# Optimization experiments

Measured on AMD Instinct MI355X. Metric: run time of the kernel, lower is better.

Reference implementation:

```python
import jax, jax.numpy as jnp
import numpy as np

H, W = 256, 256
S, S_IDX, END_BIAS = 48, 3, 10
E_IDX = S - END_BIAS          # 38
N_ITER = E_IDX - (S_IDX + 1)  # 34 sequential segments after the start segment
OUT_WIN = 10                  # outlier1d window length
OUT_THRESH = 2.0


def setup_inputs() -> dict:
    key = jax.random.key(0)
    # (x, y) event coordinates in [0, W) x [0, H); t/p/b columns are unused by the module.
    events = jax.random.uniform(key, (16, 960000, 2), jnp.float32, minval=0.0, maxval=256.0)
    return {"events": events}


def _blur(a):
    """5x5 uniform (0.04) blur, SAME padding; a: [B, S, D] -> [B, S, D]."""
    k = jnp.full((1, 1, 5, 5), 0.04, jnp.float32)
    return jax.lax.conv_general_dilated(a[:, None], k, (1, 1), [(2, 2), (2, 2)])[:, 0]


def _outlier_flags(m):
    """outlier1d(m[b, si:si+10], thresh=2)[0] for si in [S_IDX+1, E_IDX). m: [B,S] -> bool [B,N_ITER]."""
    widx = (jnp.arange(N_ITER)[:, None] + S_IDX + 1) + jnp.arange(OUT_WIN)[None, :]
    w = m[:, widx]                                   # [B, N_ITER, 10]
    med = jnp.median(w, axis=-1, keepdims=True)
    diff = jnp.abs(w - med)
    mad = jnp.median(diff, axis=-1)                  # [B, N_ITER]
    return 0.6745 * diff[..., 0] / mad > OUT_THRESH


def reference(events):
    B, N, _ = events.shape
    segmentLen = N // S            # static python int
    Nu = segmentLen * S
    x = events[:, :Nu, 0].astype(jnp.int32)   # [B, Nu]
    y = events[:, :Nu, 1].astype(jnp.int32)
    chunks = jnp.repeat(jnp.arange(S), segmentLen)   # segment id per event, [Nu]
    bidx = jnp.arange(B)[:, None]

    # per-batch x-t / y-t histograms via scatter-add
    alongX = jnp.zeros((B, S, W), jnp.float32).at[bidx, chunks[None, :], x].add(1.0)
    alongY = jnp.zeros((B, S, H), jnp.float32).at[bidx, chunks[None, :], y].add(1.0)

    def proc_axis(along, D):
        flat = along.reshape(B, -1)
        cv = (flat.mean(-1) + 3.0 * jnp.std(flat, axis=-1, ddof=1))[:, None, None]
        a = _blur(jnp.clip(along, 0.0, cv))
        m = jnp.einsum('bsd,d->bs', a, jnp.arange(D, dtype=jnp.float32)) / segmentLen
        start = m[:, S_IDX:S_IDX + 1]
        aligned = jnp.round(m - start - (D // 2 - start)).astype(jnp.int32)
        return m, aligned

    meanX, alignedX = proc_axis(alongX, W)
    meanY, alignedY = proc_axis(alongY, H)
    is_out = _outlier_flags(meanX) | _outlier_flags(meanY)   # [B, N_ITER]

    def per_batch(xb, yb, aX, aY, outb):
        xs = jnp.clip(xb - aX[chunks], 0, W - 1)
        ys = jnp.clip(yb - aY[chunks], 0, H - 1)
        idx_c = (xs + W * ys).reshape(S, segmentLen)
        idx_v = (xs // 2 + (W // 2) * (ys // 2)).reshape(S, segmentLen)
        container0 = jnp.zeros(W * H, jnp.int32).at[idx_c[S_IDX]].add(1)
        ver0 = jnp.zeros((W // 2) * (H // 2), bool).at[idx_v[S_IDX]].set(True)

        def step(carry, inp):
            container, ver, stopped = carry
            ic, iv, is_o = inp
            ver_new = ver.at[iv].set(True)
            cnt = jnp.sum(ver_new).astype(jnp.float32)
            new_info = jnp.sum(jnp.logical_xor(ver_new, ver)).astype(jnp.float32)
            brk = new_info / cnt < 0.1
            do = (~stopped) & (~is_o) & (~brk)
            stopped = stopped | ((~stopped) & (~is_o) & brk)
            container = jnp.where(do, container.at[ic].add(1), container)
            ver = jnp.where(do, ver_new, ver)
            return (container, ver, stopped), None

        (container, _, _), _ = jax.lax.scan(
            step, (container0, ver0, jnp.array(False)),
            (idx_c[S_IDX + 1:E_IDX], idx_v[S_IDX + 1:E_IDX], outb))
        c = container.astype(jnp.float32)
        cv = c.mean() + 3.0 * jnp.std(c, ddof=1)
        return jnp.clip(c, 0.0, cv) / cv

    containers = jax.vmap(per_batch)(x, y, alignedX, alignedY, is_out)  # [B, W*H]
    return containers.reshape(B, 1, H, W)
```

## Files before the change

kernel.cpp:

```cpp
#include <hip/hip_runtime.h>

#define NB 16
#define NEV 960000
#define NS 48
#define SEG 20000
#define S_IDX 3
#define E_IDX 38
#define N_ITER 34
#define ND 256
#define NCH 35

__device__ inline void centroid_pl(const float* __restrict__ along,
                                   float cv, int sI, int lane,
                                   float* mf_out, int* ai_out) {
    float vals[4][5];
    #pragma unroll
    for (int k = 0; k < 4; ++k) {
        int d = lane + 64 * k;
        #pragma unroll
        for (int ds = -2; ds <= 2; ++ds) {
            int ss = sI + ds;
            vals[k][ds + 2] = (ss >= 0 && ss < NS) ? along[ss * ND + d] : 0.0f;
        }
    }
    double acc = 0.0;
    #pragma unroll
    for (int k = 0; k < 4; ++k) {
        int d = lane + 64 * k;
        int lo = d - 2 < 0 ? 0 : d - 2;
        int hi = d + 2 > 255 ? 255 : d + 2;
        double Wd = 0.5 * (double)(lo + hi) * (double)(hi - lo + 1);
        double t = 0.0;
        #pragma unroll
        for (int ds = -2; ds <= 2; ++ds) {
            int ss = sI + ds;
            if (ss >= 0 && ss < NS) t += (double)fminf(vals[k][ds + 2], cv);
        }
        acc += t * Wd;
    }
    for (int off = 32; off; off >>= 1) acc += __shfl_down(acc, off);
    float mf = (float)(acc * 0.04 / (double)SEG);
    *mf_out = mf;
    *ai_out = (int)rintf(mf - 128.0f);
}

__device__ inline float cv_from_sums(const unsigned long long* __restrict__ cvsums,
                                     int b, int axis) {
    double ts  = 960000.0;
    double ts2 = (double)cvsums[b * 2 + axis];
    const double N = (double)(NS * ND);
    double mean = ts / N;
    double var  = (ts2 - ts * ts / N) / (N - 1.0);
    return (float)(mean + 3.0 * sqrt(var));
}

__global__ __launch_bounds__(256) void hist_kernel(const float* __restrict__ events,
                                                   float* __restrict__ alongX,
                                                   float* __restrict__ alongY,
                                                   unsigned* __restrict__ compact,
                                                   unsigned* __restrict__ container,
                                                   unsigned* __restrict__ masks,
                                                   unsigned long long* __restrict__ cvsums) {
    __shared__ unsigned hx[4][ND], hy[4][ND];
    __shared__ unsigned long long qredX[4], qredY[4];
    int tid = threadIdx.x;
    int blk = blockIdx.x;
    int b = blk / NS, c = blk % NS;
    int wave = tid >> 6, lane = tid & 63;
    #pragma unroll
    for (int j = 0; j < 4; j++) { hx[j][tid] = 0; hy[j][tid] = 0; }
    {
        uint4 z = {0u, 0u, 0u, 0u};
        for (int i = blk * 256 + tid; i < 262144; i += NB * NS * 256)
            ((uint4*)container)[i] = z;
        for (int i = blk * 256 + tid; i < 71680; i += NB * NS * 256)
            ((uint4*)masks)[i] = z;
        if (blk == 0 && tid < NB * 2) cvsums[tid] = 0ull;
    }
    __syncthreads();
    size_t base = (size_t)b * NEV + (size_t)c * SEG;
    const float4* ev4 = (const float4*)(events + base * 2);
    bool wr = (c >= S_IDX && c < E_IDX);
    uint4* dst = wr ? (uint4*)(compact + ((size_t)b * NCH + (c - S_IDX)) * (SEG / 2)) : nullptr;
    unsigned* HX = hx[wave];
    unsigned* HY = hy[wave];
    for (int k = tid; k < SEG / 8; k += 256) {
        float4 v0 = ev4[4 * k], v1 = ev4[4 * k + 1], v2 = ev4[4 * k + 2], v3 = ev4[4 * k + 3];
        int x0 = (int)v0.x, y0 = (int)v0.y, x1 = (int)v0.z, y1 = (int)v0.w;
        int x2 = (int)v1.x, y2 = (int)v1.y, x3 = (int)v1.z, y3 = (int)v1.w;
        int x4 = (int)v2.x, y4 = (int)v2.y, x5 = (int)v2.z, y5 = (int)v2.w;
        int x6 = (int)v3.x, y6 = (int)v3.y, x7 = (int)v3.z, y7 = (int)v3.w;
        x0 = x0 > 255 ? 255 : x0; y0 = y0 > 255 ? 255 : y0;
        x1 = x1 > 255 ? 255 : x1; y1 = y1 > 255 ? 255 : y1;
        x2 = x2 > 255 ? 255 : x2; y2 = y2 > 255 ? 255 : y2;
        x3 = x3 > 255 ? 255 : x3; y3 = y3 > 255 ? 255 : y3;
        x4 = x4 > 255 ? 255 : x4; y4 = y4 > 255 ? 255 : y4;
        x5 = x5 > 255 ? 255 : x5; y5 = y5 > 255 ? 255 : y5;
        x6 = x6 > 255 ? 255 : x6; y6 = y6 > 255 ? 255 : y6;
        x7 = x7 > 255 ? 255 : x7; y7 = y7 > 255 ? 255 : y7;
        atomicAdd(&HX[x0], 1u); atomicAdd(&HY[y0], 1u);
        atomicAdd(&HX[x1], 1u); atomicAdd(&HY[y1], 1u);
        atomicAdd(&HX[x2], 1u); atomicAdd(&HY[y2], 1u);
        atomicAdd(&HX[x3], 1u); atomicAdd(&HY[y3], 1u);
        atomicAdd(&HX[x4], 1u); atomicAdd(&HY[y4], 1u);
        atomicAdd(&HX[x5], 1u); atomicAdd(&HY[y5], 1u);
        atomicAdd(&HX[x6], 1u); atomicAdd(&HY[y6], 1u);
        atomicAdd(&HX[x7], 1u); atomicAdd(&HY[y7], 1u);
        if (wr) {
            uint4 p;
            p.x = (unsigned)(x0 | (y0 << 8)) | ((unsigned)(x1 | (y1 << 8)) << 16);
            p.y = (unsigned)(x2 | (y2 << 8)) | ((unsigned)(x3 | (y3 << 8)) << 16);
            p.z = (unsigned)(x4 | (y4 << 8)) | ((unsigned)(x5 | (y5 << 8)) << 16);
            p.w = (unsigned)(x6 | (y6 << 8)) | ((unsigned)(x7 | (y7 << 8)) << 16);
            dst[k] = p;
        }
    }
    __syncthreads();
    unsigned sx = hx[0][tid] + hx[1][tid] + hx[2][tid] + hx[3][tid];
    unsigned sy = hy[0][tid] + hy[1][tid] + hy[2][tid] + hy[3][tid];
    int o = (b * NS + c) * ND + tid;
    alongX[o] = (float)sx;
    alongY[o] = (float)sy;
    unsigned long long qx = (unsigned long long)sx * sx;
    unsigned long long qy = (unsigned long long)sy * sy;
    for (int off = 32; off; off >>= 1) { qx += __shfl_down(qx, off); qy += __shfl_down(qy, off); }
    if (lane == 0) { qredX[wave] = qx; qredY[wave] = qy; }
    __syncthreads();
    if (tid == 0) {
        atomicAdd(&cvsums[b * 2],     qredX[0] + qredX[1] + qredX[2] + qredX[3]);
        atomicAdd(&cvsums[b * 2 + 1], qredY[0] + qredY[1] + qredY[2] + qredY[3]);
    }
}

__global__ __launch_bounds__(256) void mask_kernel(const unsigned* __restrict__ compact,
                                                   const float* __restrict__ alongX,
                                                   const float* __restrict__ alongY,
                                                   const unsigned long long* __restrict__ cvsums,
                                                   unsigned* __restrict__ masks) {
    __shared__ unsigned sm[512];
    __shared__ int sal[2];
    int tid = threadIdx.x, blk = blockIdx.x;
    int hi = blk & 1;
    int tile = blk >> 1;
    int b = tile / NCH, ci = tile % NCH, si = S_IDX + ci;
    int wave = tid >> 6, lane = tid & 63;
    sm[tid] = 0; sm[tid + 256] = 0;
    if (wave < 2) {
        const float* along = (wave ? alongY : alongX) + (size_t)b * NS * ND;
        float cv = cv_from_sums(cvsums, b, wave);
        float mf; int ai;
        centroid_pl(along, cv, si, lane, &mf, &ai);
        if (lane == 0) sal[wave] = ai;
    }
    __syncthreads();
    int aX = sal[0], aY = sal[1];
    const uint4* cp = (const uint4*)(compact + ((size_t)b * NCH + ci) * (SEG / 2));
    for (int i = hi * 1250 + tid; i < (hi + 1) * 1250; i += 256) {
        uint4 w = cp[i];
        unsigned wsv[4] = {w.x, w.y, w.z, w.w};
        #pragma unroll
        for (int j = 0; j < 4; j++) {
            unsigned v = wsv[j];
            #pragma unroll
            for (int h = 0; h < 2; h++) {
                unsigned e = (h ? (v >> 16) : v) & 0xFFFFu;
                int xs = (int)(e & 255u) - aX; xs = xs < 0 ? 0 : (xs > 255 ? 255 : xs);
                int ys = (int)(e >> 8)   - aY; ys = ys < 0 ? 0 : (ys > 255 ? 255 : ys);
                int iv = (xs >> 1) | ((ys >> 1) << 7);
                atomicOr(&sm[iv >> 5], 1u << (iv & 31));
            }
        }
    }
    __syncthreads();
    unsigned* mo = masks + (size_t)tile * 512;
    unsigned v0 = sm[tid], v1 = sm[tid + 256];
    if (v0) atomicOr(&mo[tid], v0);
    if (v1) atomicOr(&mo[tid + 256], v1);
}

__device__ inline float median10(const float* v) {
    float w[10];
    #pragma unroll
    for (int i = 0; i < 10; i++) w[i] = v[i];
    #pragma unroll
    for (int i = 1; i < 10; i++) {
        float k = w[i]; int j = i - 1;
        while (j >= 0 && w[j] > k) { w[j + 1] = w[j]; j--; }
        w[j + 1] = k;
    }
    return 0.5f * (w[4] + w[5]);
}

__device__ inline bool outlier_flag(const float* w) {
    float med = median10(w);
    float d[10];
    #pragma unroll
    for (int i = 0; i < 10; i++) d[i] = fabsf(w[i] - med);
    float d0 = d[0];
    float mad = median10(d);
    return (0.6745f * d0 / mad) > 2.0f;
}

__device__ inline unsigned wave_sum_u32(unsigned v) {
    for (int off = 32; off; off >>= 1) v += __shfl_xor(v, off);
    return v;
}

__global__ __launch_bounds__(256) void decide_kernel(const unsigned* __restrict__ masks,
                                                     const float* __restrict__ alongX,
                                                     const float* __restrict__ alongY,
                                                     const unsigned long long* __restrict__ cvsums,
                                                     int* __restrict__ alignedX,
                                                     int* __restrict__ alignedY,
                                                     unsigned long long* __restrict__ commitmask) {
    __shared__ float mlds[2 * NS];
    int b = blockIdx.x, tid = threadIdx.x;
    int wave = tid >> 6, lane = tid & 63;
    float cv0 = cv_from_sums(cvsums, b, 0);
    float cv1 = cv_from_sums(cvsums, b, 1);
    for (int q = 0; q < 24; ++q) {
        int p = wave + 4 * q;
        int ax = p >= NS;
        int sI = p - NS * ax;
        const float* along = (ax ? alongY : alongX) + (size_t)b * NS * ND;
        float mf; int ai;
        centroid_pl(along, ax ? cv1 : cv0, sI, lane, &mf, &ai);
        if (lane == 0) {
            mlds[ax * NS + sI] = mf;
            (ax ? alignedY : alignedX)[b * NS + sI] = ai;
        }
    }
    __syncthreads();
    if (tid < 64) {
        const unsigned* mb = masks + (size_t)b * NCH * 512;
        uint4 v0 = ((const uint4*)mb)[lane * 2];
        uint4 v1 = ((const uint4*)mb)[lane * 2 + 1];
        const uint4* pp = (const uint4*)(mb + 512);
        uint4 p0 = pp[lane * 2], p1 = pp[lane * 2 + 1];
        bool f = false;
        if (lane < N_ITER) {
            const float* mx = &mlds[0];
            const float* my = &mlds[NS];
            f = outlier_flag(&mx[S_IDX + 1 + lane]) || outlier_flag(&my[S_IDX + 1 + lane]);
        }
        unsigned long long omask = __ballot(f);
        unsigned ver[8] = {v0.x, v0.y, v0.z, v0.w, v1.x, v1.y, v1.z, v1.w};
        unsigned pc = 0;
        #pragma unroll
        for (int j = 0; j < 8; j++) pc += __popc(ver[j]);
        unsigned cnt = wave_sum_u32(pc);
        unsigned long long cm = 1ull;
        for (int idx = 1; idx < NCH; ++idx) {
            uint4 c0 = p0, c1 = p1;
            if (idx + 1 < NCH) {
                const uint4* np = (const uint4*)(mb + (size_t)(idx + 1) * 512);
                p0 = np[lane * 2]; p1 = np[lane * 2 + 1];
            }
            unsigned del[8] = {c0.x, c0.y, c0.z, c0.w, c1.x, c1.y, c1.z, c1.w};
            unsigned nl = 0;
            #pragma unroll
            for (int j = 0; j < 8; j++) nl += __popc(del[j] & ~ver[j]);
            unsigned ni = wave_sum_u32(nl);
            bool is_o = (omask >> (idx - 1)) & 1;
            if (!is_o) {
                unsigned cn = cnt + ni;
                float ratio = (float)ni / (float)cn;
                if (ratio < 0.1f) break;
                cm |= 1ull << idx;
                cnt = cn;
                #pragma unroll
                for (int j = 0; j < 8; j++) ver[j] |= del[j];
            }
        }
        if (lane == 0) commitmask[b] = cm;
    }
}

__global__ __launch_bounds__(256) void commit_kernel(const unsigned* __restrict__ compact,
                                                     const int* __restrict__ alignedX,
                                                     const int* __restrict__ alignedY,
                                                     const unsigned long long* __restrict__ commitmask,
                                                     unsigned* __restrict__ container) {
    int blk = blockIdx.x, tid = threadIdx.x;
    int qi = blk & 3;
    int tile = blk >> 2;
    int b = tile / NCH, ci = tile % NCH;
    if (!((commitmask[b] >> ci) & 1ull)) return;
    int si = S_IDX + ci;
    int aX = alignedX[b * NS + si], aY = alignedY[b * NS + si];
    unsigned* cont = container + (size_t)b * 65536;
    const uint4* cp = (const uint4*)(compact + ((size_t)b * NCH + ci) * (SEG / 2));
    for (int i = qi * 625 + tid; i < (qi + 1) * 625; i += 256) {
        uint4 w = cp[i];
        unsigned wsv[4] = {w.x, w.y, w.z, w.w};
        #pragma unroll
        for (int j = 0; j < 4; j++) {
            unsigned v = wsv[j];
            #pragma unroll
            for (int h = 0; h < 2; h++) {
                unsigned e = (h ? (v >> 16) : v) & 0xFFFFu;
                int xs = (int)(e & 255u) - aX; xs = xs < 0 ? 0 : (xs > 255 ? 255 : xs);
                int ys = (int)(e >> 8)   - aY; ys = ys < 0 ? 0 : (ys > 255 ? 255 : ys);
                atomicAdd(&cont[xs | (ys << 8)], 1u);
            }
        }
    }
}

__global__ __launch_bounds__(1024) void cvfinish_kernel(const unsigned* __restrict__ container,
                                                        float* __restrict__ out) {
    __shared__ unsigned long long sA[16], sB[16];
    __shared__ float cvs;
    int b = blockIdx.x, tid = threadIdx.x;
    const uint4* c4 = (const uint4*)(container + (size_t)b * 65536);
    unsigned long long s = 0, s2 = 0;
    for (int i = tid; i < 16384; i += 1024) {
        uint4 v = c4[i];
        s  += (unsigned long long)v.x + v.y + v.z + v.w;
        s2 += (unsigned long long)v.x * v.x + (unsigned long long)v.y * v.y
            + (unsigned long long)v.z * v.z + (unsigned long long)v.w * v.w;
    }
    for (int off = 32; off; off >>= 1) { s += __shfl_down(s, off); s2 += __shfl_down(s2, off); }
    if ((tid & 63) == 0) { sA[tid >> 6] = s; sB[tid >> 6] = s2; }
    __syncthreads();
    if (tid == 0) {
        unsigned long long S = 0, S2 = 0;
        #pragma unroll
        for (int w = 0; w < 16; w++) { S += sA[w]; S2 += sB[w]; }
        double ts  = (double)S;
        double ts2 = (double)S2;
        double mean = ts / 65536.0;
        double var  = (ts2 - ts * ts / 65536.0) / 65535.0;
        cvs = (float)(mean + 3.0 * sqrt(var));
    }
    __syncthreads();
    float cv = cvs;
    float4* o4 = (float4*)out + (size_t)b * 16384;
    for (int i = tid; i < 16384; i += 1024) {
        uint4 v = c4[i];
        float4 o;
        o.x = fminf((float)v.x, cv) / cv;
        o.y = fminf((float)v.y, cv) / cv;
        o.z = fminf((float)v.z, cv) / cv;
        o.w = fminf((float)v.w, cv) / cv;
        o4[i] = o;
    }
}

extern "C" void kernel_launch(void* const* d_in, const int* in_sizes, int n_in,
                              void* d_out, int out_size, void* d_ws, size_t ws_size,
                              hipStream_t stream) {
    const float* events = (const float*)d_in[0];
    float* out = (float*)d_out;
    char* ws = (char*)d_ws;

    float*    alongX    = (float*)(ws);
    float*    alongY    = (float*)(ws + 786432);
    unsigned* container = (unsigned*)(ws + 1572864);
    int*      alignedX  = (int*)(ws + 5767168);
    int*      alignedY  = (int*)(ws + 5770240);
    unsigned long long* commitmask = (unsigned long long*)(ws + 5779456);
    unsigned long long* cvsums     = (unsigned long long*)(ws + 5779840);
    unsigned* compact   = (unsigned*)(ws + 6291456);
    unsigned* masks     = (unsigned*)(ws + 29360128);

    hist_kernel<<<NB * NS, 256, 0, stream>>>(events, alongX, alongY, compact,
                                             container, masks, cvsums);
    mask_kernel<<<NB * NCH * 2, 256, 0, stream>>>(compact, alongX, alongY, cvsums, masks);
    decide_kernel<<<NB, 256, 0, stream>>>(masks, alongX, alongY, cvsums,
                                          alignedX, alignedY, commitmask);
    commit_kernel<<<NB * NCH * 4, 256, 0, stream>>>(compact, alignedX, alignedY,
                                                    commitmask, container);
    cvfinish_kernel<<<NB, 1024, 0, stream>>>(container, out);
}
```

Baseline: 298.9 us.

## Coalesce histogram event loads and widen parallelism of decide and finalize stages

In the histogram kernel, each thread now loads four float4s spaced a quarter-segment apart instead of four consecutive ones, so neighbouring lanes read neighbouring addresses. This only changes which events a thread handles; the histograms and later stages do not depend on event order. The decide kernel runs with 1024 threads per block so the 96 centroid rows are spread over 16 waves instead of 4. The single 16-block finalize kernel becomes two launches: a 256-block partial sum/sum-of-squares reduction using 64-bit atomics, then a 1024-block elementwise clip-and-normalize. This trades an extra launch and an atomic buffer for much more occupancy on the tail.

```diff
diff --git a/kernel.cpp b/kernel.cpp
--- a/kernel.cpp
+++ b/kernel.cpp
@@ -60,7 +60,8 @@
                                                    unsigned* __restrict__ compact,
                                                    unsigned* __restrict__ container,
                                                    unsigned* __restrict__ masks,
-                                                   unsigned long long* __restrict__ cvsums) {
+                                                   unsigned long long* __restrict__ cvsums,
+                                                   unsigned long long* __restrict__ sums) {
     __shared__ unsigned hx[4][ND], hy[4][ND];
     __shared__ unsigned long long qredX[4], qredY[4];
     int tid = threadIdx.x;
@@ -76,6 +77,7 @@
         for (int i = blk * 256 + tid; i < 71680; i += NB * NS * 256)
             ((uint4*)masks)[i] = z;
         if (blk == 0 && tid < NB * 2) cvsums[tid] = 0ull;
+        if (blk == 1 && tid < NB * 2) sums[tid] = 0ull;
     }
     __syncthreads();
     size_t base = (size_t)b * NEV + (size_t)c * SEG;
@@ -85,7 +87,7 @@
     unsigned* HX = hx[wave];
     unsigned* HY = hy[wave];
     for (int k = tid; k < SEG / 8; k += 256) {
-        float4 v0 = ev4[4 * k], v1 = ev4[4 * k + 1], v2 = ev4[4 * k + 2], v3 = ev4[4 * k + 3];
+        float4 v0 = ev4[k], v1 = ev4[2500 + k], v2 = ev4[5000 + k], v3 = ev4[7500 + k];
         int x0 = (int)v0.x, y0 = (int)v0.y, x1 = (int)v0.z, y1 = (int)v0.w;
         int x2 = (int)v1.x, y2 = (int)v1.y, x3 = (int)v1.z, y3 = (int)v1.w;
         int x4 = (int)v2.x, y4 = (int)v2.y, x5 = (int)v2.z, y5 = (int)v2.w;
@@ -206,20 +208,21 @@
     return v;
 }
 
-__global__ __launch_bounds__(256) void decide_kernel(const unsigned* __restrict__ masks,
-                                                     const float* __restrict__ alongX,
-                                                     const float* __restrict__ alongY,
-                                                     const unsigned long long* __restrict__ cvsums,
-                                                     int* __restrict__ alignedX,
-                                                     int* __restrict__ alignedY,
-                                                     unsigned long long* __restrict__ commitmask) {
+__global__ __launch_bounds__(1024) void decide_kernel(const unsigned* __restrict__ masks,
+                                                      const float* __restrict__ alongX,
+                                                      const float* __restrict__ alongY,
+                                                      const unsigned long long* __restrict__ cvsums,
+                                                      int* __restrict__ alignedX,
+                                                      int* __restrict__ alignedY,
+                                                      unsigned long long* __restrict__ commitmask) {
     __shared__ float mlds[2 * NS];
     int b = blockIdx.x, tid = threadIdx.x;
     int wave = tid >> 6, lane = tid & 63;
     float cv0 = cv_from_sums(cvsums, b, 0);
     float cv1 = cv_from_sums(cvsums, b, 1);
-    for (int q = 0; q < 24; ++q) {
-        int p = wave + 4 * q;
+    #pragma unroll
+    for (int q = 0; q < 6; ++q) {
+        int p = wave + 16 * q;
         int ax = p >= NS;
         int sI = p - NS * ax;
         const float* along = (ax ? alongY : alongX) + (size_t)b * NS * ND;
@@ -307,44 +310,45 @@
     }
 }
 
-__global__ __launch_bounds__(1024) void cvfinish_kernel(const unsigned* __restrict__ container,
-                                                        float* __restrict__ out) {
-    __shared__ unsigned long long sA[16], sB[16];
-    __shared__ float cvs;
-    int b = blockIdx.x, tid = threadIdx.x;
-    const uint4* c4 = (const uint4*)(container + (size_t)b * 65536);
+__global__ __launch_bounds__(256) void cv_kernel(const unsigned* __restrict__ container,
+                                                 unsigned long long* __restrict__ sums) {
+    __shared__ unsigned long long sredA[4], sredB[4];
+    int tid = threadIdx.x, blk = blockIdx.x;
+    int b = blk >> 4, part = blk & 15;
+    const uint4* c4 = (const uint4*)(container + (size_t)b * 65536) + part * 1024;
     unsigned long long s = 0, s2 = 0;
-    for (int i = tid; i < 16384; i += 1024) {
+    for (int i = tid; i < 1024; i += 256) {
         uint4 v = c4[i];
         s  += (unsigned long long)v.x + v.y + v.z + v.w;
         s2 += (unsigned long long)v.x * v.x + (unsigned long long)v.y * v.y
             + (unsigned long long)v.z * v.z + (unsigned long long)v.w * v.w;
     }
     for (int off = 32; off; off >>= 1) { s += __shfl_down(s, off); s2 += __shfl_down(s2, off); }
-    if ((tid & 63) == 0) { sA[tid >> 6] = s; sB[tid >> 6] = s2; }
+    if ((tid & 63) == 0) { sredA[tid >> 6] = s; sredB[tid >> 6] = s2; }
     __syncthreads();
     if (tid == 0) {
-        unsigned long long S = 0, S2 = 0;
-        #pragma unroll
-        for (int w = 0; w < 16; w++) { S += sA[w]; S2 += sB[w]; }
-        double ts  = (double)S;
-        double ts2 = (double)S2;
-        double mean = ts / 65536.0;
-        double var  = (ts2 - ts * ts / 65536.0) / 65535.0;
-        cvs = (float)(mean + 3.0 * sqrt(var));
-    }
-    __syncthreads();
-    float cv = cvs;
-    float4* o4 = (float4*)out + (size_t)b * 16384;
-    for (int i = tid; i < 16384; i += 1024) {
-        uint4 v = c4[i];
-        float4 o;
-        o.x = fminf((float)v.x, cv) / cv;
-        o.y = fminf((float)v.y, cv) / cv;
-        o.z = fminf((float)v.z, cv) / cv;
-        o.w = fminf((float)v.w, cv) / cv;
-        o4[i] = o;
-    }
+        atomicAdd(&sums[b * 2],     sredA[0] + sredA[1] + sredA[2] + sredA[3]);
+        atomicAdd(&sums[b * 2 + 1], sredB[0] + sredB[1] + sredB[2] + sredB[3]);
+    }
+}
+
+__global__ __launch_bounds__(256) void finish_kernel(const unsigned* __restrict__ container,
+                                                     const unsigned long long* __restrict__ sums,
+                                                     float* __restrict__ out) {
+    int g = blockIdx.x * 256 + threadIdx.x;
+    int b = g >> 14;
+    double ts  = (double)sums[b * 2];
+    double ts2 = (double)sums[b * 2 + 1];
+    double mean = ts / 65536.0;
+    double var  = (ts2 - ts * ts / 65536.0) / 65535.0;
+    float cv = (float)(mean + 3.0 * sqrt(var));
+    uint4 v = ((const uint4*)container)[g];
+    float4 o;
+    o.x = fminf((float)v.x, cv) / cv;
+    o.y = fminf((float)v.y, cv) / cv;
+    o.z = fminf((float)v.z, cv) / cv;
+    o.w = fminf((float)v.w, cv) / cv;
+    ((float4*)out)[g] = o;
 }
 
 extern "C" void kernel_launch(void* const* d_in, const int* in_sizes, int n_in,
@@ -360,16 +364,18 @@
     int*      alignedX  = (int*)(ws + 5767168);
     int*      alignedY  = (int*)(ws + 5770240);
     unsigned long long* commitmask = (unsigned long long*)(ws + 5779456);
+    unsigned long long* sums       = (unsigned long long*)(ws + 5779584);
     unsigned long long* cvsums     = (unsigned long long*)(ws + 5779840);
     unsigned* compact   = (unsigned*)(ws + 6291456);
     unsigned* masks     = (unsigned*)(ws + 29360128);
 
     hist_kernel<<<NB * NS, 256, 0, stream>>>(events, alongX, alongY, compact,
-                                             container, masks, cvsums);
+                                             container, masks, cvsums, sums);
     mask_kernel<<<NB * NCH * 2, 256, 0, stream>>>(compact, alongX, alongY, cvsums, masks);
-    decide_kernel<<<NB, 256, 0, stream>>>(masks, alongX, alongY, cvsums,
-                                          alignedX, alignedY, commitmask);
+    decide_kernel<<<NB, 1024, 0, stream>>>(masks, alongX, alongY, cvsums,
+                                           alignedX, alignedY, commitmask);
     commit_kernel<<<NB * NCH * 4, 256, 0, stream>>>(compact, alignedX, alignedY,
                                                     commitmask, container);
-    cvfinish_kernel<<<NB, 1024, 0, stream>>>(container, out);
-}
+    cv_kernel<<<NB * 16, 256, 0, stream>>>(container, sums);
+    finish_kernel<<<1024, 256, 0, stream>>>(container, sums, out);
+}
```

New measurement: 268.7 us. 1.11x faster.
